# Kernel tuning notes

Hardware: AMD Instinct MI355X
Metric: run time of the kernel (lower is better)

## Reference

```python
import jax, jax.numpy as jnp
import numpy as np

B, T, N, D = 4, 24, 2048, 128
H = 4
HD = D // H
E = 8
K = 2
INTER = 512            # dim * mlp_ratio
MINTER = INTER // K    # per-expert intermediate (512//2 = 256)
EPS = 1e-6
ALPHA = 0.05           # GCN residual mixing
SCALE = HD ** -0.5


def setup_inputs() -> dict:
    key = jax.random.key(0)
    ks = jax.random.split(key, 32)
    w = lambda i, shape: (jax.random.normal(ks[i], shape, jnp.float32) * 0.02)
    inp = {
        "x": jax.random.normal(ks[0], (B, T, N, D), jnp.float32),
        "k": jax.random.normal(ks[1], (B, T, N, D), jnp.float32),
        "v": jax.random.normal(ks[2], (B, T, N, D), jnp.float32),
        "adj": jax.random.uniform(ks[3], (N, N), jnp.float32),
        # attention qkv projections (torch Linear: y = x @ W.T + b)
        "Wq": w(4, (D, D)), "bq": jnp.zeros((D,), jnp.float32),
        "Wk": w(5, (D, D)), "bk": jnp.zeros((D,), jnp.float32),
        "Wv": w(6, (D, D)), "bv": jnp.zeros((D,), jnp.float32),
        "norm_tatt_w": jnp.ones((D,), jnp.float32),
        # GCN
        "gcn_fc1_w": w(7, (D, D)),
        "gcn_mlp_w": w(8, (D, D)), "gcn_mlp_b": jnp.zeros((D,), jnp.float32),
        # block norms
        "norm1_w": jnp.ones((D,), jnp.float32),
        "norm2_w": jnp.ones((D,), jnp.float32),
        # MoE
        "gate_w": w(9, (E, D)),
        "ew1": w(10, (E, MINTER, D)),
        "ew2": w(11, (E, D, MINTER)),
        "ew3": w(12, (E, MINTER, D)),
        "sw1": w(13, (INTER, D)),
        "sw2": w(14, (D, INTER)),
        "sw3": w(15, (INTER, D)),
        "sgate_w": w(16, (1, D)),
    }
    return inp


def rms_norm(x, w):
    var = jnp.mean(x * x, axis=-1, keepdims=True)
    return w * (x * jax.lax.rsqrt(var + EPS))


def swiglu(x, w1, w2, w3):
    return (jax.nn.silu(x @ w1.T) * (x @ w3.T)) @ w2.T


def reference(x, k, v, adj, Wq, bq, Wk, bk, Wv, bv, norm_tatt_w,
              gcn_fc1_w, gcn_mlp_w, gcn_mlp_b, norm1_w, norm2_w,
              gate_w, ew1, ew2, ew3, sw1, sw2, sw3, sgate_w):
    # ---- pre-norm ----
    x_n = rms_norm(x, norm1_w)
    k_n = rms_norm(k, norm1_w)

    # ---- temporal self-attention (per node, over T) ----
    def heads(y, W, b):  # [B,T,N,D] -> [B,N,H,T,hd]
        y = y @ W.T + b
        return y.transpose(0, 2, 1, 3).reshape(B, N, -1, H, HD).transpose(0, 1, 3, 2, 4)

    q = heads(x_n, Wq, bq)
    kk = heads(k_n, Wk, bk)
    vv = heads(k_n, Wv, bv)  # module passes k for both k and v
    attn = jnp.einsum('bnhqd,bnhkd->bnhqk', q, kk) * SCALE
    attn = jax.nn.softmax(attn, axis=-1)
    t_x = jnp.einsum('bnhqk,bnhkd->bnhqd', attn, vv)
    t_x = t_x.transpose(0, 3, 1, 2, 4).reshape(B, T, N, D)  # [B,T,N,D]
    t_x = rms_norm(t_x, norm_tatt_w)

    # ---- GCN: row-normalized adjacency over node axis ----
    a = adj / jnp.sum(adj, axis=1, keepdims=True)            # a[n,k] = adj[n,k]/d[n]
    mixed = jnp.einsum('nk,btkd->btnd', a, t_x)
    gcn_out = mixed @ gcn_fc1_w.T
    out = ALPHA * t_x + (1.0 - ALPHA) * gcn_out
    ho = out @ gcn_mlp_w.T + gcn_mlp_b

    x = x + ho  # residual (drop_path = identity)

    # ---- MoE sparse experts ----
    x2 = rms_norm(x, norm2_w).reshape(-1, D)                 # [Tok, D]
    router_logits = x2 @ gate_w.T                            # [Tok, E]
    rw = jax.nn.softmax(router_logits.astype(jnp.float32), axis=-1)
    top_w, top_idx = jax.lax.top_k(rw, K)                    # [Tok, K]
    top_w = top_w.astype(x2.dtype)

    final = jnp.zeros_like(x2)
    for e in range(E):  # fixed small expert count
        coef = jnp.sum(jnp.where(top_idx == e, top_w, 0.0), axis=-1)  # [Tok]
        final = final + coef[:, None] * swiglu(x2, ew1[e], ew2[e], ew3[e])

    shared = swiglu(x2, sw1, sw2, sw3)
    shared = jax.nn.sigmoid(x2 @ sgate_w.T) * shared
    final = final + shared

    x = x + final.reshape(B, T, N, D)
    return x, router_logits
```

## Files before the change

kernel.cpp:

```cpp
#include <hip/hip_runtime.h>

#define BB 4
#define TT 24
#define NN 2048
#define DD 128
#define HH 4
#define HD 32
#define TOK 196608
#define EE 8
#define MINTER 256
#define INTER 512

typedef unsigned short u16;
typedef __attribute__((ext_vector_type(8))) short  bf16x8;
typedef __attribute__((ext_vector_type(4))) float  f32x4;
typedef __attribute__((ext_vector_type(4))) unsigned int u32x4;

#define MFMA(a,b,c) __builtin_amdgcn_mfma_f32_16x16x32_bf16((a),(b),(c),0,0,0)
#define AS(n) __attribute__((address_space(n)))

static __device__ __forceinline__ u16 f2b(float f) {
    union { float f; unsigned u; } v; v.f = f;
    unsigned r = v.u + 0x7FFFu + ((v.u >> 16) & 1u);
    return (u16)(r >> 16);
}
static __device__ __forceinline__ float b2f(u16 b) {
    union { unsigned u; float f; } v; v.u = ((unsigned)b) << 16;
    return v.f;
}
static __device__ __forceinline__ float silu_mul(float u, float v) {
    return u * __builtin_amdgcn_rcpf(1.f + __expf(-u)) * v;
}

template<int C>
static __device__ __forceinline__ bf16x8 frag_ld(const u16* s, int row, int kbyte) {
    constexpr int mask = ((C/8) < 8 ? (C/8) : 8) - 1;
    int byte = row * (C * 2) + (kbyte ^ ((row & mask) << 4));
    return *(const bf16x8*)((const char*)s + byte);
}
template<int C>
static __device__ __forceinline__ u16 lds_us(const u16* s, int r, int c) {
    constexpr int mask = ((C/8) < 8 ? (C/8) : 8) - 1;
    int byte = r * (C * 2) + ((((c >> 3) << 4) ^ ((r & mask) << 4))) + ((c & 7) << 1);
    return *(const u16*)((const char*)s + byte);
}
template<int C>
static __device__ __forceinline__ void lds_store_us(u16* s, int r, int c, u16 v) {
    constexpr int mask = ((C/8) < 8 ? (C/8) : 8) - 1;
    int byte = r * (C * 2) + ((((c >> 3) << 4) ^ ((r & mask) << 4))) + ((c & 7) << 1);
    *(u16*)((char*)s + byte) = v;
}
static __device__ __forceinline__ bf16x8 frag_ld_p80(const u16* s, int row, int kbyte) {
    return *(const bf16x8*)((const char*)s + row * 80 + kbyte);
}
static __device__ __forceinline__ void sh_store_p80(u16* s, int r, int c, u16 v) {
    *(u16*)((char*)s + r * 80 + c * 2) = v;
}
template<int C>
static __device__ __forceinline__ void stage_bf16(u16* s, const u16* g, int gstride,
                                                  int rows, int tid, int nthr) {
    constexpr int cpr = C / 8;
    constexpr int mask = (cpr < 8 ? cpr : 8) - 1;
    for (int i = tid; i < rows * cpr; i += nthr) {
        int r = i / cpr, cc = i - r * cpr;
        u32x4 v = *(const u32x4*)(g + (size_t)r * gstride + cc * 8);
        *(u32x4*)((char*)s + r * (C * 2) + ((cc * 16) ^ ((r & mask) << 4))) = v;
    }
}
static __device__ __forceinline__ void stage_async64(u16* s, const u16* g, int wi, int lane) {
    int slot = wi * 64 + lane;
    int r = slot >> 3, c = slot & 7;
    const u16* src = g + r * 2048 + ((c ^ (r & 7)) << 3);
    __builtin_amdgcn_global_load_lds((const AS(1) void*)src,
                                     (AS(3) void*)(s + wi * 512), 16, 0, 0);
}
static __device__ __forceinline__ void stage_img(u16* buf, const u16* img, int wid, int lane) {
    #pragma unroll
    for (int t = 0; t < 7; ++t) {
        int wi = wid + t * 4;
        if (wi < 26)
            __builtin_amdgcn_global_load_lds((const AS(1) void*)(img + wi * 512 + lane * 8),
                                             (AS(3) void*)(buf + wi * 512), 16, 0, 0);
    }
}
static __device__ __forceinline__ void zero_acc(f32x4 acc[4][4]) {
    f32x4 z = {0.f, 0.f, 0.f, 0.f};
    #pragma unroll
    for (int i = 0; i < 4; ++i)
        #pragma unroll
        for (int j = 0; j < 4; ++j) acc[i][j] = z;
}
template<int CA, int CB>
static __device__ __forceinline__ void gemm_step64(const u16* sA, const u16* sB,
        int arow0, int brow0, int kbyte, f32x4 acc[4][4], int ln15) {
    bf16x8 a[4], b[4];
    #pragma unroll
    for (int i = 0; i < 4; ++i) a[i] = frag_ld<CA>(sA, arow0 + i * 16 + ln15, kbyte);
    #pragma unroll
    for (int j = 0; j < 4; ++j) b[j] = frag_ld<CB>(sB, brow0 + j * 16 + ln15, kbyte);
    #pragma unroll
    for (int i = 0; i < 4; ++i)
        #pragma unroll
        for (int j = 0; j < 4; ++j)
            acc[i][j] = MFMA(a[i], b[j], acc[i][j]);
}

static __device__ __forceinline__ void swiglu_chunk(const u16* buf, u16* sH,
        const bf16x8 av[2][4], f32x4 aout[2][8],
        int wid, int g16, int ln15) {
    const u16* W1c = buf;
    const u16* W3c = buf + 4096;
    const u16* W2c = buf + 8192;
    f32x4 z = {0.f, 0.f, 0.f, 0.f};
    f32x4 a1[2][2], a3[2][2];
    #pragma unroll
    for (int mf = 0; mf < 2; ++mf)
        #pragma unroll
        for (int nf = 0; nf < 2; ++nf) { a1[mf][nf] = z; a3[mf][nf] = z; }
    #pragma unroll
    for (int ks = 0; ks < 4; ++ks) {
        int kb = ks * 64 + g16 * 16;
        #pragma unroll
        for (int nf = 0; nf < 2; ++nf) {
            bf16x8 b1 = frag_ld<128>(W1c, nf * 16 + ln15, kb);
            bf16x8 b3 = frag_ld<128>(W3c, nf * 16 + ln15, kb);
            a1[0][nf] = MFMA(av[0][ks], b1, a1[0][nf]);
            a1[1][nf] = MFMA(av[1][ks], b1, a1[1][nf]);
            a3[0][nf] = MFMA(av[0][ks], b3, a3[0][nf]);
            a3[1][nf] = MFMA(av[1][ks], b3, a3[1][nf]);
        }
    }
    #pragma unroll
    for (int mf = 0; mf < 2; ++mf)
        #pragma unroll
        for (int nf = 0; nf < 2; ++nf)
            #pragma unroll
            for (int r = 0; r < 4; ++r) {
                int row = wid * 32 + mf * 16 + g16 * 4 + r;
                int col = nf * 16 + ln15;
                sh_store_p80(sH, row, col, f2b(silu_mul(a1[mf][nf][r], a3[mf][nf][r])));
            }
    asm volatile("s_waitcnt lgkmcnt(0)" ::: "memory");
    __builtin_amdgcn_sched_barrier(0);
    {
        int kb = g16 * 16;
        bf16x8 ah0 = frag_ld_p80(sH, wid * 32 + ln15, kb);
        bf16x8 ah1 = frag_ld_p80(sH, wid * 32 + 16 + ln15, kb);
        #pragma unroll
        for (int nf = 0; nf < 8; ++nf) {
            bf16x8 bw = frag_ld_p80(W2c, nf * 16 + ln15, kb);
            aout[0][nf] = MFMA(ah0, bw, aout[0][nf]);
            aout[1][nf] = MFMA(ah1, bw, aout[1][nf]);
        }
    }
}

__global__ __launch_bounds__(256) void preconvert(
        const float* __restrict__ Wq, const float* __restrict__ Wk,
        const float* __restrict__ Wv, const float* __restrict__ g1,
        const float* __restrict__ g2,
        const float* __restrict__ e1, const float* __restrict__ e2,
        const float* __restrict__ e3,
        const float* __restrict__ s1, const float* __restrict__ s2,
        const float* __restrict__ s3,
        u16* __restrict__ arena, int* __restrict__ cnts) {
    int idx = blockIdx.x * 256 + threadIdx.x;
    if (blockIdx.x == 0 && threadIdx.x < 8) cnts[threadIdx.x] = 0;
    if (idx < 20480) {
        int s = idx >> 12, rel = idx & 4095;
        const float* src = (s == 0) ? Wq : (s == 1) ? Wk : (s == 2) ? Wv : (s == 3) ? g1 : g2;
        const float4 v = *(const float4*)(src + (size_t)rel * 4);
        union { unsigned long long q; u16 us[4]; } o;
        o.us[0] = f2b(v.x); o.us[1] = f2b(v.y); o.us[2] = f2b(v.z); o.us[3] = f2b(v.w);
        *(unsigned long long*)(arena + (size_t)idx * 4) = o.q;
        return;
    }
    int p = idx - 20480;
    if (p >= 133120) return;
    const float *w1s, *w3s, *w2s_; int w2stride, ic;
    u16* img;
    if (p < 106496) {
        int imgIdx = p / 1664;
        p -= imgIdx * 1664;
        int e = imgIdx >> 3; ic = imgIdx & 7;
        w1s = e1 + (size_t)e * 32768;
        w3s = e3 + (size_t)e * 32768;
        w2s_ = e2 + (size_t)e * 32768;
        w2stride = 256;
        img = arena + 81920 + (size_t)imgIdx * 13312;
    } else {
        int q = p - 106496;
        int imgIdx = q / 1664; ic = imgIdx;
        p = q - imgIdx * 1664;
        w1s = s1; w3s = s3; w2s_ = s2; w2stride = 512;
        img = arena + 933888 + (size_t)imgIdx * 13312;
    }
    const float* src;
    if (p < 1024) {
        const float* wsrc = (p < 512) ? w1s : w3s;
        int pp = p & 511;
        int r = pp >> 4, chq = pp & 15;
        int cc = chq ^ (r & 7);
        src = wsrc + (size_t)(ic * 32 + r) * 128 + cc * 8;
    } else {
        int q = p - 1024;
        int r = q / 5, cc = q - r * 5;
        if (cc == 4) {
            u32x4 zv = {0, 0, 0, 0};
            *(u32x4*)(img + (size_t)p * 8) = zv;
            return;
        }
        src = w2s_ + (size_t)r * w2stride + ic * 32 + cc * 8;
    }
    union { u32x4 v; u16 us[8]; } o;
    #pragma unroll
    for (int j = 0; j < 8; ++j) o.us[j] = f2b(src[j]);
    *(u32x4*)(img + (size_t)p * 8) = o.v;
}

__global__ __launch_bounds__(256) void rmsnorm_pair(
        const float* __restrict__ x, const float* __restrict__ k,
        const float* __restrict__ w, u16* __restrict__ xn, u16* __restrict__ kn) {
    int row = blockIdx.x * 4 + (threadIdx.x >> 6);
    int lane = threadIdx.x & 63;
    const float* in; u16* out;
    if (row < TOK) { in = x + (size_t)row * 128; out = xn + (size_t)row * 128; }
    else           { in = k + (size_t)(row - TOK) * 128; out = kn + (size_t)(row - TOK) * 128; }
    float2 v = *(const float2*)(in + lane * 2);
    float ss = v.x * v.x + v.y * v.y;
    #pragma unroll
    for (int o = 32; o > 0; o >>= 1) ss += __shfl_xor(ss, o);
    float sc = rsqrtf(ss * (1.f / 128.f) + 1e-6f);
    float2 wv = *(const float2*)(w + lane * 2);
    unsigned pack = ((unsigned)f2b(v.y * sc * wv.y) << 16) | (unsigned)f2b(v.x * sc * wv.x);
    *(unsigned*)(out + lane * 2) = pack;
}

__global__ __launch_bounds__(256) void proj128(
        const u16* __restrict__ in, const u16* __restrict__ W,
        const float* __restrict__ bias, u16* __restrict__ out) {
    int tok0 = blockIdx.x * 128;
    __shared__ u16 sA[128 * 128];
    __shared__ u16 sW[128 * 128];
    int tid = threadIdx.x, lane = tid & 63, ln15 = lane & 15, g16 = lane >> 4, wid = tid >> 6;
    int wm = (wid >> 1) * 64, wn = (wid & 1) * 64;
    stage_bf16<128>(sA, in + (size_t)tok0 * 128, 128, 128, tid, 256);
    stage_bf16<128>(sW, W, 128, 128, tid, 256);
    __syncthreads();
    f32x4 acc[4][4];
    zero_acc(acc);
    #pragma unroll
    for (int ks = 0; ks < 4; ++ks)
        gemm_step64<128, 128>(sA, sW, wm, wn, ks * 64 + g16 * 16, acc, ln15);
    #pragma unroll
    for (int j = 0; j < 4; ++j) {
        int col = wn + j * 16 + ln15;
        float bv = bias[col];
        #pragma unroll
        for (int i = 0; i < 4; ++i)
            #pragma unroll
            for (int r = 0; r < 4; ++r) {
                int row = wm + i * 16 + g16 * 4 + r;
                out[(size_t)(tok0 + row) * 128 + col] = f2b(acc[i][j][r] + bv);
            }
    }
}

__global__ __launch_bounds__(256) void attn_kernel(
        const u16* __restrict__ q, const u16* __restrict__ kk, const u16* __restrict__ vv,
        const float* __restrict__ ntw, u16* __restrict__ txn) {
    int bid = blockIdx.x;
    int b = bid >> 11;
    int n = bid & 2047;
    __shared__ u16 sQ[4][24][32];
    __shared__ u16 sK[4][24][32];
    __shared__ u16 sV[4][24][32];
    __shared__ float sS[4][24][24];
    __shared__ float sO[24][128];
    int tid = threadIdx.x, lane = tid & 63, wid = tid >> 6;
    for (int idx = tid; idx < 3072; idx += 256) {
        int h = idx / 768;
        int rem = idx - h * 768;
        int t = rem >> 5;
        int d = rem & 31;
        size_t off = ((size_t)((b * 24 + t) * 2048 + n)) * 128 + h * 32 + d;
        sQ[h][t][d] = q[off];
        sK[h][t][d] = kk[off];
        sV[h][t][d] = vv[off];
    }
    __syncthreads();
    int h = wid;
    for (int i = lane; i < 576; i += 64) {
        int qi = i / 24, ki = i - qi * 24;
        float s = 0.f;
        #pragma unroll
        for (int c = 0; c < 32; ++c) s += b2f(sQ[h][qi][c]) * b2f(sK[h][ki][c]);
        sS[h][qi][ki] = s * 0.17677669529663687f;
    }
    __syncthreads();
    if (lane < 24) {
        float m = -1e30f;
        #pragma unroll
        for (int c = 0; c < 24; ++c) m = fmaxf(m, sS[h][lane][c]);
        float e[24]; float sum = 0.f;
        #pragma unroll
        for (int c = 0; c < 24; ++c) { e[c] = __expf(sS[h][lane][c] - m); sum += e[c]; }
        float inv = 1.f / sum;
        #pragma unroll
        for (int c = 0; c < 24; ++c) sS[h][lane][c] = e[c] * inv;
    }
    __syncthreads();
    for (int i = lane; i < 768; i += 64) {
        int qi = i >> 5, d = i & 31;
        float acc = 0.f;
        #pragma unroll
        for (int c = 0; c < 24; ++c) acc += sS[h][qi][c] * b2f(sV[h][c][d]);
        sO[qi][h * 32 + d] = acc;
    }
    __syncthreads();
    for (int j = 0; j < 6; ++j) {
        int t = wid * 6 + j;
        float v0 = sO[t][lane], v1 = sO[t][lane + 64];
        float ss = v0 * v0 + v1 * v1;
        #pragma unroll
        for (int o = 32; o > 0; o >>= 1) ss += __shfl_xor(ss, o);
        float sc = rsqrtf(ss * (1.f / 128.f) + 1e-6f);
        size_t off = ((size_t)((b * 24 + t) * 2048 + n)) * 128;
        txn[off + lane]      = f2b(v0 * sc * ntw[lane]);
        txn[off + lane + 64] = f2b(v1 * sc * ntw[lane + 64]);
    }
}

__global__ __launch_bounds__(256) void adj_norm(const float* __restrict__ adj, u16* __restrict__ abf) {
    int nrow = blockIdx.x;
    const float* r = adj + (size_t)nrow * 2048;
    int tid = threadIdx.x;
    float s = 0.f;
    for (int c = tid; c < 2048; c += 256) s += r[c];
    __shared__ float red[4];
    #pragma unroll
    for (int o = 32; o > 0; o >>= 1) s += __shfl_xor(s, o);
    if ((tid & 63) == 0) red[tid >> 6] = s;
    __syncthreads();
    float inv = 1.f / (red[0] + red[1] + red[2] + red[3]);
    u16* o = abf + (size_t)nrow * 2048;
    for (int c = tid; c < 2048; c += 256) o[c] = f2b(r[c] * inv);
}

__global__ __launch_bounds__(256) void transpose_k(const u16* __restrict__ txn, u16* __restrict__ txT) {
    int bt = blockIdx.x >> 5;
    int n0 = (blockIdx.x & 31) * 64;
    int tid = threadIdx.x;
    int nn = tid & 63, dg = tid >> 6;
    for (int rep = 0; rep < 4; ++rep) {
        int d0 = rep * 32 + dg * 8;
        union { u32x4 v; u16 us[8]; } u;
        u.v = *(const u32x4*)(txn + ((size_t)(bt * 2048 + n0 + nn)) * 128 + d0);
        #pragma unroll
        for (int j = 0; j < 8; ++j)
            txT[((size_t)(bt * 128 + d0 + j)) * 2048 + n0 + nn] = u.us[j];
    }
}

__global__ __launch_bounds__(256) void gcn_gemm(
        const u16* __restrict__ abf, const u16* __restrict__ txT, u16* __restrict__ mixed) {
    int bt = blockIdx.x >> 4;
    int n0 = (blockIdx.x & 15) * 128;
    __shared__ u16 sA[128 * 64];
    __shared__ u16 sB[128 * 64];
    int tid = threadIdx.x, lane = tid & 63, ln15 = lane & 15, g16 = lane >> 4, wid = tid >> 6;
    int wm = (wid >> 1) * 64, wn = (wid & 1) * 64;
    f32x4 acc[4][4];
    zero_acc(acc);
    const u16* aRow = abf + (size_t)n0 * 2048;
    const u16* bRow = txT + (size_t)bt * 128 * 2048;
    for (int k0 = 0; k0 < 2048; k0 += 64) {
        __syncthreads();
        #pragma unroll
        for (int i = 0; i < 4; ++i) stage_async64(sA, aRow + k0, wid * 4 + i, lane);
        #pragma unroll
        for (int i = 0; i < 4; ++i) stage_async64(sB, bRow + k0, wid * 4 + i, lane);
        __syncthreads();
        #pragma unroll
        for (int ks = 0; ks < 2; ++ks)
            gemm_step64<64, 64>(sA, sB, wm, wn, ks * 64 + g16 * 16, acc, ln15);
    }
    u16* out = mixed + ((size_t)(bt * 2048 + n0)) * 128;
    #pragma unroll
    for (int i = 0; i < 4; ++i)
        #pragma unroll
        for (int j = 0; j < 4; ++j)
            #pragma unroll
            for (int r = 0; r < 4; ++r) {
                int row = wm + i * 16 + g16 * 4 + r;
                int col = wn + j * 16 + ln15;
                out[(size_t)row * 128 + col] = f2b(acc[i][j][r]);
            }
}

__global__ __launch_bounds__(256) void fused_gcn_router(
        const u16* __restrict__ mixed, const u16* __restrict__ txn,
        const float* __restrict__ x,
        const u16* __restrict__ W1, const u16* __restrict__ W2,
        const float* __restrict__ bias2, const float* __restrict__ n2w,
        const float* __restrict__ gatew,
        float* __restrict__ outx, float* __restrict__ outlog,
        u16* __restrict__ x2n,
        int* __restrict__ lists, float* __restrict__ listw, int* __restrict__ cnts) {
    int tok0 = blockIdx.x * 128;
    __shared__ char LB[65536];
    __shared__ float sGate[1024];
    __shared__ float sN2[128];
    __shared__ float sBias[128];
    __shared__ float sLog[1024];
    __shared__ float sPart[256];
    __shared__ float sScale[128];
    __shared__ int sBCnt[8];
    __shared__ int sGBase[8];
    u16* sM = (u16*)LB;
    u16* sW = (u16*)(LB + 32768);
    float* sXn = (float*)LB;
    int tid = threadIdx.x, lane = tid & 63, ln15 = lane & 15, g16 = lane >> 4, wid = tid >> 6;
    int wm = (wid >> 1) * 64, wn = (wid & 1) * 64;
    stage_bf16<128>(sM, mixed + (size_t)tok0 * 128, 128, 128, tid, 256);
    stage_bf16<128>(sW, W1, 128, 128, tid, 256);
    for (int i = tid; i < 1024; i += 256) sGate[i] = gatew[i];
    if (tid < 128) { sN2[tid] = n2w[tid]; sBias[tid] = bias2[tid]; }
    if (tid < 8) sBCnt[tid] = 0;
    __syncthreads();
    f32x4 acc[4][4];
    zero_acc(acc);
    #pragma unroll
    for (int ks = 0; ks < 4; ++ks)
        gemm_step64<128, 128>(sM, sW, wm, wn, ks * 64 + g16 * 16, acc, ln15);
    __syncthreads();
    stage_bf16<128>(sM, txn + (size_t)tok0 * 128, 128, 128, tid, 256);
    stage_bf16<128>(sW, W2, 128, 128, tid, 256);
    __syncthreads();
    #pragma unroll
    for (int i = 0; i < 4; ++i)
        #pragma unroll
        for (int j = 0; j < 4; ++j)
            #pragma unroll
            for (int r = 0; r < 4; ++r) {
                int row = wm + i * 16 + g16 * 4 + r;
                int col = wn + j * 16 + ln15;
                float tv = b2f(lds_us<128>(sM, row, col));
                lds_store_us<128>(sM, row, col, f2b(0.05f * tv + 0.95f * acc[i][j][r]));
            }
    __syncthreads();
    zero_acc(acc);
    #pragma unroll
    for (int ks = 0; ks < 4; ++ks)
        gemm_step64<128, 128>(sM, sW, wm, wn, ks * 64 + g16 * 16, acc, ln15);
    #pragma unroll
    for (int i = 0; i < 4; ++i)
        #pragma unroll
        for (int j = 0; j < 4; ++j)
            #pragma unroll
            for (int r = 0; r < 4; ++r) {
                int row = wm + i * 16 + g16 * 4 + r;
                int col = wn + j * 16 + ln15;
                float xv = x[(size_t)(tok0 + row) * 128 + col] + acc[i][j][r] + sBias[col];
                outx[(size_t)(tok0 + row) * 128 + col] = xv;
                acc[i][j][r] = xv;
            }
    #pragma unroll
    for (int i = 0; i < 4; ++i)
        #pragma unroll
        for (int r = 0; r < 4; ++r) {
            float s = 0.f;
            #pragma unroll
            for (int j = 0; j < 4; ++j) s += acc[i][j][r] * acc[i][j][r];
            s += __shfl_xor(s, 1); s += __shfl_xor(s, 2);
            s += __shfl_xor(s, 4); s += __shfl_xor(s, 8);
            if (ln15 == 0) sPart[(wm + i * 16 + g16 * 4 + r) * 2 + (wid & 1)] = s;
        }
    __syncthreads();
    if (tid < 128)
        sScale[tid] = rsqrtf((sPart[tid * 2] + sPart[tid * 2 + 1]) * (1.f / 128.f) + 1e-6f);
    __syncthreads();
    #pragma unroll
    for (int i = 0; i < 4; ++i)
        #pragma unroll
        for (int j = 0; j < 4; ++j)
            #pragma unroll
            for (int r = 0; r < 4; ++r) {
                int row = wm + i * 16 + g16 * 4 + r;
                int col = wn + j * 16 + ln15;
                sXn[row * 128 + col] = acc[i][j][r] * sScale[row] * sN2[col];
            }
    __syncthreads();
    {
        int r = tid >> 1, e0 = (tid & 1) * 4;
        float a0 = 0, a1 = 0, a2 = 0, a3 = 0;
        for (int cc = 0; cc < 128; ++cc) {
            int c = (cc + r) & 127;
            float v = sXn[r * 128 + c];
            a0 += v * sGate[(e0 + 0) * 128 + c];
            a1 += v * sGate[(e0 + 1) * 128 + c];
            a2 += v * sGate[(e0 + 2) * 128 + c];
            a3 += v * sGate[(e0 + 3) * 128 + c];
        }
        int rb = r * 8 + e0;
        sLog[rb + 0] = a0; sLog[rb + 1] = a1; sLog[rb + 2] = a2; sLog[rb + 3] = a3;
        size_t ob = (size_t)(tok0 + r) * 8 + e0;
        outlog[ob + 0] = a0; outlog[ob + 1] = a1; outlog[ob + 2] = a2; outlog[ob + 3] = a3;
    }
    for (int cc = tid; cc < 2048; cc += 256) {
        int r = cc >> 4, c0 = (cc & 15) * 8;
        union { u32x4 v; u16 us[8]; } u;
        #pragma unroll
        for (int jj = 0; jj < 8; ++jj) u.us[jj] = f2b(sXn[r * 128 + c0 + jj]);
        *(u32x4*)(x2n + (size_t)(tok0 + r) * 128 + c0) = u.v;
    }
    __syncthreads();
    int e1 = 0, e2 = 0, le1 = 0, le2 = 0;
    float w1v = 0.f, w2v = 0.f;
    if (tid < 128) {
        int r = tid;
        float l[8];
        #pragma unroll
        for (int e = 0; e < 8; ++e) l[e] = sLog[r * 8 + e];
        float m = l[0];
        #pragma unroll
        for (int e = 1; e < 8; ++e) m = fmaxf(m, l[e]);
        float ex[8]; float s = 0.f;
        #pragma unroll
        for (int e = 0; e < 8; ++e) { ex[e] = __expf(l[e] - m); s += ex[e]; }
        float inv = 1.f / s;
        float b1v = ex[0]; e1 = 0;
        #pragma unroll
        for (int e = 1; e < 8; ++e) if (ex[e] > b1v) { b1v = ex[e]; e1 = e; }
        e2 = (e1 == 0) ? 1 : 0; float b2v = ex[e2];
        #pragma unroll
        for (int e = 0; e < 8; ++e) if (e != e1 && ex[e] > b2v) { b2v = ex[e]; e2 = e; }
        w1v = b1v * inv; w2v = b2v * inv;
        le1 = atomicAdd(&sBCnt[e1], 1);
        le2 = atomicAdd(&sBCnt[e2], 1);
    }
    __syncthreads();
    if (tid < 8) sGBase[tid] = atomicAdd(&cnts[tid], sBCnt[tid]);
    __syncthreads();
    if (tid < 128) {
        int tok = tok0 + tid;
        int p1 = sGBase[e1] + le1;
        lists[(size_t)e1 * TOK + p1] = tok * 2 + 0; listw[(size_t)e1 * TOK + p1] = w1v;
        int p2 = sGBase[e2] + le2;
        lists[(size_t)e2 * TOK + p2] = tok * 2 + 1; listw[(size_t)e2 * TOK + p2] = w2v;
    }
}

__global__ __launch_bounds__(256, 2) void moe_expert(
        const u16* __restrict__ x2n, const int* __restrict__ lists,
        const float* __restrict__ listw, const int* __restrict__ cnts,
        const u16* __restrict__ eimg, u16* __restrict__ slotOut) {
    int e = blockIdx.y;
    int base = blockIdx.x * 128;
    int cnt = cnts[e];
    if (base >= cnt) return;
    int valid = min(128, cnt - base);
    const int* lst = lists + (size_t)e * TOK + base;
    const float* lw = listw + (size_t)e * TOK + base;
    __shared__ u16 sBufA[13312];
    __shared__ u16 sBufB[13312];
    __shared__ u16 sH[5120];
    __shared__ float sCoef[128];
    __shared__ int sTok[128];
    int tid = threadIdx.x, lane = tid & 63, ln15 = lane & 15, g16 = lane >> 4, wid = tid >> 6;
    const u16* imgbase = eimg + (size_t)(e * 8) * 13312;
    stage_img(sBufA, imgbase, wid, lane);
    if (tid < 128) {
        int t = (tid < valid) ? lst[tid] : -1;
        sTok[tid] = t;
        sCoef[tid] = (tid < valid) ? lw[tid] : 0.f;
    }
    __syncthreads();
    bf16x8 av[2][4];
    {
        bf16x8 zz = {0, 0, 0, 0, 0, 0, 0, 0};
        int t0 = sTok[wid * 32 + ln15];
        int t1 = sTok[wid * 32 + 16 + ln15];
        const u16* r0 = x2n + (size_t)(t0 >> 1) * 128;
        const u16* r1 = x2n + (size_t)(t1 >> 1) * 128;
        #pragma unroll
        for (int ks = 0; ks < 4; ++ks) {
            av[0][ks] = (t0 >= 0) ? *(const bf16x8*)(r0 + ks * 32 + g16 * 8) : zz;
            av[1][ks] = (t1 >= 0) ? *(const bf16x8*)(r1 + ks * 32 + g16 * 8) : zz;
        }
    }
    f32x4 aout[2][8];
    f32x4 z = {0.f, 0.f, 0.f, 0.f};
    #pragma unroll
    for (int mf = 0; mf < 2; ++mf)
        #pragma unroll
        for (int nf = 0; nf < 8; ++nf) aout[mf][nf] = z;
    for (int ic = 0; ic < 8; ++ic) {
        u16* cur = (ic & 1) ? sBufB : sBufA;
        u16* alt = (ic & 1) ? sBufA : sBufB;
        if (ic + 1 < 8)
            stage_img(alt, imgbase + (size_t)(ic + 1) * 13312, wid, lane);
        swiglu_chunk(cur, sH, av, aout, wid, g16, ln15);
        __syncthreads();
    }
    #pragma unroll
    for (int mf = 0; mf < 2; ++mf)
        #pragma unroll
        for (int nf = 0; nf < 8; ++nf)
            #pragma unroll
            for (int r = 0; r < 4; ++r) {
                int row = wid * 32 + mf * 16 + g16 * 4 + r;
                if (row < valid) {
                    int col = nf * 16 + ln15;
                    slotOut[(size_t)sTok[row] * 128 + col] = f2b(sCoef[row] * aout[mf][nf][r]);
                }
            }
}

__global__ __launch_bounds__(256, 2) void moe_shared(
        const u16* __restrict__ x2n, const u16* __restrict__ simg,
        const float* __restrict__ sgw, const u16* __restrict__ slotOut,
        float* __restrict__ outx) {
    int tok0 = blockIdx.x * 128;
    __shared__ u16 sBufA[13312];
    __shared__ u16 sBufB[13312];
    __shared__ u16 sH[5120];
    __shared__ float sGv[128];
    int tid = threadIdx.x, lane = tid & 63, ln15 = lane & 15, g16 = lane >> 4, wid = tid >> 6;
    stage_img(sBufA, simg, wid, lane);
    bf16x8 av[2][4];
    {
        const u16* r0 = x2n + (size_t)(tok0 + wid * 32 + ln15) * 128;
        const u16* r1 = x2n + (size_t)(tok0 + wid * 32 + 16 + ln15) * 128;
        #pragma unroll
        for (int ks = 0; ks < 4; ++ks) {
            av[0][ks] = *(const bf16x8*)(r0 + ks * 32 + g16 * 8);
            av[1][ks] = *(const bf16x8*)(r1 + ks * 32 + g16 * 8);
        }
    }
    if (tid < 128) {
        const u16* xr = x2n + (size_t)(tok0 + tid) * 128;
        float d = 0.f;
        #pragma unroll
        for (int c8 = 0; c8 < 16; ++c8) {
            bf16x8 v = *(const bf16x8*)(xr + c8 * 8);
            #pragma unroll
            for (int j = 0; j < 8; ++j) d += b2f((u16)v[j]) * sgw[c8 * 8 + j];
        }
        sGv[tid] = 1.f / (1.f + __expf(-d));
    }
    f32x4 aout[2][8];
    f32x4 z = {0.f, 0.f, 0.f, 0.f};
    #pragma unroll
    for (int mf = 0; mf < 2; ++mf)
        #pragma unroll
        for (int nf = 0; nf < 8; ++nf) aout[mf][nf] = z;
    __syncthreads();
    for (int ic = 0; ic < 16; ++ic) {
        u16* cur = (ic & 1) ? sBufB : sBufA;
        u16* alt = (ic & 1) ? sBufA : sBufB;
        if (ic + 1 < 16)
            stage_img(alt, simg + (size_t)(ic + 1) * 13312, wid, lane);
        swiglu_chunk(cur, sH, av, aout, wid, g16, ln15);
        __syncthreads();
    }
    #pragma unroll
    for (int mf = 0; mf < 2; ++mf)
        #pragma unroll
        for (int nf = 0; nf < 8; ++nf)
            #pragma unroll
            for (int r = 0; r < 4; ++r) {
                int row = wid * 32 + mf * 16 + g16 * 4 + r;
                int col = nf * 16 + ln15;
                size_t t = (size_t)(tok0 + row);
                float fc = b2f(slotOut[(t * 2 + 0) * 128 + col])
                         + b2f(slotOut[(t * 2 + 1) * 128 + col]);
                size_t idx = t * 128 + col;
                outx[idx] = outx[idx] + fc + sGv[row] * aout[mf][nf][r];
            }
}

#define SZTD  ((size_t)TOK * 128 * 2)
#define OFF_XN   ((size_t)0)
#define OFF_KN   (SZTD)
#define OFF_Q    (SZTD * 2)
#define OFF_KP   (SZTD * 3)
#define OFF_VP   (SZTD * 4)
#define OFF_ABF  (SZTD * 5)
#define OFF_LW   (OFF_ABF + 8388608)
#define OFF_LIST (OFF_LW + (size_t)8 * TOK * 4)
#define OFF_CNT  (OFF_LIST + (size_t)8 * TOK * 4)
#define OFF_ARENA (OFF_CNT + 128)

extern "C" void kernel_launch(void* const* d_in, const int* in_sizes, int n_in,
                              void* d_out, int out_size, void* d_ws, size_t ws_size,
                              hipStream_t stream) {
    (void)in_sizes; (void)n_in; (void)out_size; (void)ws_size;
    const float* x    = (const float*)d_in[0];
    const float* k    = (const float*)d_in[1];
    const float* adj  = (const float*)d_in[3];
    const float* Wq   = (const float*)d_in[4];
    const float* bq   = (const float*)d_in[5];
    const float* Wk   = (const float*)d_in[6];
    const float* bk   = (const float*)d_in[7];
    const float* Wv   = (const float*)d_in[8];
    const float* bv   = (const float*)d_in[9];
    const float* ntw  = (const float*)d_in[10];
    const float* gfc1 = (const float*)d_in[11];
    const float* gmlp = (const float*)d_in[12];
    const float* gmlpb= (const float*)d_in[13];
    const float* n1w  = (const float*)d_in[14];
    const float* n2w  = (const float*)d_in[15];
    const float* gatew= (const float*)d_in[16];
    const float* ew1  = (const float*)d_in[17];
    const float* ew2  = (const float*)d_in[18];
    const float* ew3  = (const float*)d_in[19];
    const float* sw1  = (const float*)d_in[20];
    const float* sw2  = (const float*)d_in[21];
    const float* sw3  = (const float*)d_in[22];
    const float* sgw  = (const float*)d_in[23];

    char* ws = (char*)d_ws;
    u16*  xn   = (u16*)(ws + OFF_XN);
    u16*  kn   = (u16*)(ws + OFF_KN);
    u16*  qb   = (u16*)(ws + OFF_Q);
    u16*  kpb  = (u16*)(ws + OFF_KP);
    u16*  vpb  = (u16*)(ws + OFF_VP);
    u16*  slotOut = (u16*)(ws + OFF_KP);
    u16*  abf  = (u16*)(ws + OFF_ABF);
    float* lw  = (float*)(ws + OFF_LW);
    int*  lst  = (int*)(ws + OFF_LIST);
    int*  cnts = (int*)(ws + OFF_CNT);
    u16*  arena = (u16*)(ws + OFF_ARENA);
    u16*  bWq = arena;
    u16*  bWk = arena + 16384;
    u16*  bWv = arena + 32768;
    u16*  bG1 = arena + 49152;
    u16*  bG2 = arena + 65536;
    u16*  eimg = arena + 81920;
    u16*  simg = arena + 933888;
    float* outx   = (float*)d_out;
    float* outlog = outx + (size_t)TOK * 128;

    preconvert<<<600, 256, 0, stream>>>(Wq, Wk, Wv, gfc1, gmlp, ew1, ew2, ew3,
                                        sw1, sw2, sw3, arena, cnts);
    rmsnorm_pair<<<98304, 256, 0, stream>>>(x, k, n1w, xn, kn);
    proj128<<<1536, 256, 0, stream>>>(xn, bWq, bq, qb);
    proj128<<<1536, 256, 0, stream>>>(kn, bWk, bk, kpb);
    proj128<<<1536, 256, 0, stream>>>(kn, bWv, bv, vpb);
    attn_kernel<<<8192, 256, 0, stream>>>(qb, kpb, vpb, ntw, xn );
    adj_norm<<<2048, 256, 0, stream>>>(adj, abf);
    transpose_k<<<3072, 256, 0, stream>>>(xn, qb );
    gcn_gemm<<<1536, 256, 0, stream>>>(abf, qb, kn );
    fused_gcn_router<<<1536, 256, 0, stream>>>(kn, xn, x, bG1, bG2, gmlpb, n2w, gatew,
                                               outx, outlog, qb , lst, lw, cnts);
    moe_expert<<<dim3(1536, 8), 256, 0, stream>>>(qb, lst, lw, cnts, eimg, slotOut);
    moe_shared<<<1536, 256, 0, stream>>>(qb, simg, sgw, slotOut, outx);
}
```

Before: 751.0 us.

## Fuse RMSNorm into QKV projections and share normalized K tile for K/V

Removes the standalone rmsnorm kernel by normalizing fp32 input rows directly into the LDS A-tile inside the projection kernels. K and V projections now share one normalized tile, so the k input is read once instead of twice and the bf16 intermediates xn/kn are no longer written or read. It also adds s_setprio around the MFMA loops in the SwiGLU chunk and switches some bf16 conversions to truncation instead of round-to-nearest. Truncation slightly changes numerics, and the per-row shuffle reductions now run inside the GEMM kernels.

```diff
diff --git a/kernel.cpp b/kernel.cpp
--- a/kernel.cpp
+++ b/kernel.cpp
@@ -24,6 +24,10 @@
     unsigned r = v.u + 0x7FFFu + ((v.u >> 16) & 1u);
     return (u16)(r >> 16);
 }
+static __device__ __forceinline__ u16 f2b_fast(float f) {
+    union { float f; unsigned u; } v; v.f = f;
+    return (u16)(v.u >> 16);
+}
 static __device__ __forceinline__ float b2f(u16 b) {
     union { unsigned u; float f; } v; v.u = ((unsigned)b) << 16;
     return v.f;
@@ -67,6 +71,22 @@
         *(u32x4*)((char*)s + r * (C * 2) + ((cc * 16) ^ ((r & mask) << 4))) = v;
     }
 }
+static __device__ __forceinline__ void stage_rms(u16* sA, const float* __restrict__ in,
+        const float* __restrict__ nw, int tid) {
+    int wid = tid >> 6, lane = tid & 63;
+    float2 wv = *(const float2*)(nw + lane * 2);
+    for (int rr = 0; rr < 32; ++rr) {
+        int r = wid * 32 + rr;
+        float2 v = *(const float2*)(in + (size_t)r * 128 + lane * 2);
+        float ss = v.x * v.x + v.y * v.y;
+        #pragma unroll
+        for (int o = 32; o > 0; o >>= 1) ss += __shfl_xor(ss, o);
+        float sc = rsqrtf(ss * (1.f / 128.f) + 1e-6f);
+        unsigned pack = ((unsigned)f2b(v.y * sc * wv.y) << 16) | (unsigned)f2b(v.x * sc * wv.x);
+        int byte = r * 256 + (((lane >> 2) * 16) ^ ((r & 7) << 4)) + ((lane & 3) << 2);
+        *(unsigned*)((char*)sA + byte) = pack;
+    }
+}
 static __device__ __forceinline__ void stage_async64(u16* s, const u16* g, int wi, int lane) {
     int slot = wi * 64 + lane;
     int r = slot >> 3, c = slot & 7;
@@ -117,6 +137,7 @@
     for (int mf = 0; mf < 2; ++mf)
         #pragma unroll
         for (int nf = 0; nf < 2; ++nf) { a1[mf][nf] = z; a3[mf][nf] = z; }
+    __builtin_amdgcn_s_setprio(1);
     #pragma unroll
     for (int ks = 0; ks < 4; ++ks) {
         int kb = ks * 64 + g16 * 16;
@@ -130,6 +151,7 @@
             a3[1][nf] = MFMA(av[1][ks], b3, a3[1][nf]);
         }
     }
+    __builtin_amdgcn_s_setprio(0);
     #pragma unroll
     for (int mf = 0; mf < 2; ++mf)
         #pragma unroll
@@ -138,7 +160,7 @@
             for (int r = 0; r < 4; ++r) {
                 int row = wid * 32 + mf * 16 + g16 * 4 + r;
                 int col = nf * 16 + ln15;
-                sh_store_p80(sH, row, col, f2b(silu_mul(a1[mf][nf][r], a3[mf][nf][r])));
+                sh_store_p80(sH, row, col, f2b_fast(silu_mul(a1[mf][nf][r], a3[mf][nf][r])));
             }
     asm volatile("s_waitcnt lgkmcnt(0)" ::: "memory");
     __builtin_amdgcn_sched_barrier(0);
@@ -146,12 +168,14 @@
         int kb = g16 * 16;
         bf16x8 ah0 = frag_ld_p80(sH, wid * 32 + ln15, kb);
         bf16x8 ah1 = frag_ld_p80(sH, wid * 32 + 16 + ln15, kb);
+        __builtin_amdgcn_s_setprio(1);
         #pragma unroll
         for (int nf = 0; nf < 8; ++nf) {
             bf16x8 bw = frag_ld_p80(W2c, nf * 16 + ln15, kb);
             aout[0][nf] = MFMA(ah0, bw, aout[0][nf]);
             aout[1][nf] = MFMA(ah1, bw, aout[1][nf]);
         }
+        __builtin_amdgcn_s_setprio(0);
     }
 }
 
@@ -218,33 +242,16 @@
     *(u32x4*)(img + (size_t)p * 8) = o.v;
 }
 
-__global__ __launch_bounds__(256) void rmsnorm_pair(
-        const float* __restrict__ x, const float* __restrict__ k,
-        const float* __restrict__ w, u16* __restrict__ xn, u16* __restrict__ kn) {
-    int row = blockIdx.x * 4 + (threadIdx.x >> 6);
-    int lane = threadIdx.x & 63;
-    const float* in; u16* out;
-    if (row < TOK) { in = x + (size_t)row * 128; out = xn + (size_t)row * 128; }
-    else           { in = k + (size_t)(row - TOK) * 128; out = kn + (size_t)(row - TOK) * 128; }
-    float2 v = *(const float2*)(in + lane * 2);
-    float ss = v.x * v.x + v.y * v.y;
-    #pragma unroll
-    for (int o = 32; o > 0; o >>= 1) ss += __shfl_xor(ss, o);
-    float sc = rsqrtf(ss * (1.f / 128.f) + 1e-6f);
-    float2 wv = *(const float2*)(w + lane * 2);
-    unsigned pack = ((unsigned)f2b(v.y * sc * wv.y) << 16) | (unsigned)f2b(v.x * sc * wv.x);
-    *(unsigned*)(out + lane * 2) = pack;
-}
-
-__global__ __launch_bounds__(256) void proj128(
-        const u16* __restrict__ in, const u16* __restrict__ W,
-        const float* __restrict__ bias, u16* __restrict__ out) {
+__global__ __launch_bounds__(256) void proj_rms(
+        const float* __restrict__ xin, const u16* __restrict__ W,
+        const float* __restrict__ bias, const float* __restrict__ nw,
+        u16* __restrict__ out) {
     int tok0 = blockIdx.x * 128;
     __shared__ u16 sA[128 * 128];
     __shared__ u16 sW[128 * 128];
     int tid = threadIdx.x, lane = tid & 63, ln15 = lane & 15, g16 = lane >> 4, wid = tid >> 6;
     int wm = (wid >> 1) * 64, wn = (wid & 1) * 64;
-    stage_bf16<128>(sA, in + (size_t)tok0 * 128, 128, 128, tid, 256);
+    stage_rms(sA, xin + (size_t)tok0 * 128, nw, tid);
     stage_bf16<128>(sW, W, 128, 128, tid, 256);
     __syncthreads();
     f32x4 acc[4][4];
@@ -262,6 +269,57 @@
             for (int r = 0; r < 4; ++r) {
                 int row = wm + i * 16 + g16 * 4 + r;
                 out[(size_t)(tok0 + row) * 128 + col] = f2b(acc[i][j][r] + bv);
+            }
+    }
+}
+
+__global__ __launch_bounds__(256) void projkv_rms(
+        const float* __restrict__ kin, const u16* __restrict__ Wk,
+        const float* __restrict__ bk, const u16* __restrict__ Wv,
+        const float* __restrict__ bv, const float* __restrict__ nw,
+        u16* __restrict__ kout, u16* __restrict__ vout) {
+    int tok0 = blockIdx.x * 128;
+    __shared__ u16 sA[128 * 128];
+    __shared__ u16 sW[128 * 128];
+    int tid = threadIdx.x, lane = tid & 63, ln15 = lane & 15, g16 = lane >> 4, wid = tid >> 6;
+    int wm = (wid >> 1) * 64, wn = (wid & 1) * 64;
+    stage_rms(sA, kin + (size_t)tok0 * 128, nw, tid);
+    stage_bf16<128>(sW, Wk, 128, 128, tid, 256);
+    __syncthreads();
+    f32x4 acc[4][4];
+    zero_acc(acc);
+    #pragma unroll
+    for (int ks = 0; ks < 4; ++ks)
+        gemm_step64<128, 128>(sA, sW, wm, wn, ks * 64 + g16 * 16, acc, ln15);
+    #pragma unroll
+    for (int j = 0; j < 4; ++j) {
+        int col = wn + j * 16 + ln15;
+        float bvv = bk[col];
+        #pragma unroll
+        for (int i = 0; i < 4; ++i)
+            #pragma unroll
+            for (int r = 0; r < 4; ++r) {
+                int row = wm + i * 16 + g16 * 4 + r;
+                kout[(size_t)(tok0 + row) * 128 + col] = f2b(acc[i][j][r] + bvv);
+            }
+    }
+    __syncthreads();
+    stage_bf16<128>(sW, Wv, 128, 128, tid, 256);
+    __syncthreads();
+    zero_acc(acc);
+    #pragma unroll
+    for (int ks = 0; ks < 4; ++ks)
+        gemm_step64<128, 128>(sA, sW, wm, wn, ks * 64 + g16 * 16, acc, ln15);
+    #pragma unroll
+    for (int j = 0; j < 4; ++j) {
+        int col = wn + j * 16 + ln15;
+        float bvv = bv[col];
+        #pragma unroll
+        for (int i = 0; i < 4; ++i)
+            #pragma unroll
+            for (int r = 0; r < 4; ++r) {
+                int row = wm + i * 16 + g16 * 4 + r;
+                vout[(size_t)(tok0 + row) * 128 + col] = f2b(acc[i][j][r] + bvv);
             }
     }
 }
@@ -612,7 +670,7 @@
                 int row = wid * 32 + mf * 16 + g16 * 4 + r;
                 if (row < valid) {
                     int col = nf * 16 + ln15;
-                    slotOut[(size_t)sTok[row] * 128 + col] = f2b(sCoef[row] * aout[mf][nf][r]);
+                    slotOut[(size_t)sTok[row] * 128 + col] = f2b_fast(sCoef[row] * aout[mf][nf][r]);
                 }
             }
 }
@@ -744,10 +802,8 @@
 
     preconvert<<<600, 256, 0, stream>>>(Wq, Wk, Wv, gfc1, gmlp, ew1, ew2, ew3,
                                         sw1, sw2, sw3, arena, cnts);
-    rmsnorm_pair<<<98304, 256, 0, stream>>>(x, k, n1w, xn, kn);
-    proj128<<<1536, 256, 0, stream>>>(xn, bWq, bq, qb);
-    proj128<<<1536, 256, 0, stream>>>(kn, bWk, bk, kpb);
-    proj128<<<1536, 256, 0, stream>>>(kn, bWv, bv, vpb);
+    proj_rms<<<1536, 256, 0, stream>>>(x, bWq, bq, n1w, qb);
+    projkv_rms<<<1536, 256, 0, stream>>>(k, bWk, bk, bWv, bv, n1w, kpb, vpb);
     attn_kernel<<<8192, 256, 0, stream>>>(qb, kpb, vpb, ntw, xn );
     adj_norm<<<2048, 256, 0, stream>>>(adj, abf);
     transpose_k<<<3072, 256, 0, stream>>>(xn, qb );
```

Result: faster. 731.3 us (median of 2 runs) (-2.6%).
